# Performance work log

Hardware: AMD Instinct MI355X
Metric: run time of the kernel (lower is better)

## Reference

```python
import jax, jax.numpy as jnp
import numpy as np
from jax import lax

DECAY = 0.1
THRESH = 0.5
LENS = 1.0
D_IN = 2 * 34 * 34  # 2312
HID = 800
NC = 10

@jax.custom_vjp
def act_fun(x):
    return (x > THRESH).astype(x.dtype)

def _act_fwd(x):
    return act_fun(x), x

def _act_bwd(x, g):
    p = jax.nn.sigmoid((x - THRESH) / LENS)
    return (g * p * (1.0 - p) / LENS,)

act_fun.defvjp(_act_fwd, _act_bwd)


def setup_inputs() -> dict:
    key = jax.random.key(0)
    ks = jax.random.split(key, 8)
    B, T = 128, 300
    inp = jax.random.uniform(ks[0], (B, 2, 34, 34, 50), dtype=jnp.float32)
    X = jnp.zeros((B, 2, 34, 34, T), dtype=jnp.float32)
    idx = jax.random.randint(ks[1], (B,), 0, T - 50)
    W1 = jax.random.normal(ks[2], (HID, D_IN), dtype=jnp.float32) * 0.02
    b1 = jnp.zeros((HID,), dtype=jnp.float32)
    W2 = jax.random.normal(ks[3], (NC, HID), dtype=jnp.float32) * 0.03
    b2 = jnp.zeros((NC,), dtype=jnp.float32)
    Wc = jax.random.uniform(ks[4], (1, HID + 4), dtype=jnp.float32)  # ctrl init U(0,1)
    bc = jax.random.uniform(ks[5], (1,), dtype=jnp.float32)
    return {"input": inp, "X": X, "idx": idx, "W1": W1, "b1": b1,
            "W2": W2, "b2": b2, "Wc": Wc, "bc": bc}


def _paste(Xi, clip_i, idx_i):
    # X[i, :, :, :, idx:idx+50] = input[i].view(2,34,34,50)
    return lax.dynamic_update_slice(Xi, clip_i, (0, 0, 0, idx_i))


def reference(input, X, idx, W1, b1, W2, b2, Wc, bc):
    B = X.shape[0]
    T = X.shape[-1]
    X = jax.vmap(_paste)(X, input, idx.astype(jnp.int32))
    xs = jnp.moveaxis(X.reshape(B, D_IN, T), -1, 0)  # [T, B, D_IN]

    t = jnp.arange(T)
    freqs = jnp.stack([
        jnp.ones(T), (t % 2 == 0).astype(jnp.float32),
        (t % 10 == 0).astype(jnp.float32), (t % 100 == 0).astype(jnp.float32),
    ], axis=1).astype(X.dtype)  # [T, 4]
    is_first = (t == 0)

    f32 = X.dtype
    carry0 = (
        jnp.zeros((B, HID), f32), jnp.zeros((B, HID), f32),   # h1_mem, h1_spike
        jnp.zeros((B, NC), f32), jnp.zeros((B, NC), f32),     # h2_mem, h2_spike
        jnp.zeros((B, 1), f32), jnp.zeros((B, 1), f32),       # c_mem, c_spike
        jnp.ones((B, 1), f32), jnp.zeros((B, NC), f32),       # bgt, h2_sumspike
    )

    def step(carry, inps):
        h1m, h1s, h2m, h2s, cm, cs, bgt, sum2 = carry
        x, fq, first = inps
        x_a = jnp.where(first, x, x * cs)
        bgt = jnp.where(cs == 1.0, bgt + 1.0, bgt)
        h1m = h1m * DECAY * (1.0 - h1s) + x_a @ W1.T + b1
        h1s = act_fun(h1m)
        h2m = h2m * DECAY * (1.0 - h2s) + h1s @ W2.T + b2
        h2s = act_fun(h2m)
        c_in = jnp.concatenate(
            [lax.stop_gradient(h1s), jnp.broadcast_to(fq, (B, 4))], axis=1)
        cm = cm * 0.1 * (1.0 - cs) + c_in @ Wc.T + bc
        cs = act_fun(cm)
        sum2 = sum2 + h2s
        return (h1m, h1s, h2m, h2s, cm, cs, bgt, sum2), None

    carry, _ = lax.scan(step, carry0, (xs, freqs, is_first))
    bgt, sum2 = carry[6], carry[7]
    rate = sum2 / bgt
    return rate, X
```

## Files before the change

### kernel.cpp

```cpp
#include <hip/hip_runtime.h>

#define D_IN 2312
#define HID  800
#define NCLS 10
#define BATCH 128
#define TSTEPS 300
#define WIN  50

#define MT 64
#define NT 32
#define BKK 16
#define NTM 100
#define NTN 25
#define GEMM_BLOCKS (NTM * NTN)
#define BLK 128
#define RPASTE 1920
#define TOTQ (BATCH * D_IN * (TSTEPS / 4))

__global__ __launch_bounds__(BLK) void gemm_kernel(
    const float* __restrict__ inp,
    const float* __restrict__ W1,
    float*       __restrict__ P)
{
  __shared__ float As[BKK][MT];
  __shared__ float Bs[BKK][NT + 4];

  int t  = threadIdx.x;
  int bx = blockIdx.x;

  int mt = bx / NTN;
  int nt = bx - mt * NTN;
  int m0 = mt * MT, n0 = nt * NT;

  int am = t & 63;
  int ah = t >> 6;
  int r  = m0 + am;
  int bb = r / 50, ss = r - bb * 50;
  const float* aptr = inp + (size_t)bb * (D_IN * WIN) + ss;

  int bn = t >> 4;
  int bk = t & 15;

  int l  = t & 63;
  int lm = l & 7;
  int ln = l >> 3;
  int tm = ah * 32 + lm * 4;
  int tn = ln * 4;

  float aN[8], bN[4];
#pragma unroll
  for (int q = 0; q < 8; ++q) aN[q] = aptr[(ah * 8 + q) * WIN];
#pragma unroll
  for (int p = 0; p < 4; ++p)
    bN[p] = W1[(size_t)(n0 + bn + 8 * p) * D_IN + bk];

  float acc[4][4] = {};

  for (int k0 = 0; k0 < D_IN; k0 += BKK) {
#pragma unroll
    for (int q = 0; q < 8; ++q) As[ah * 8 + q][am] = aN[q];
#pragma unroll
    for (int p = 0; p < 4; ++p) Bs[bk][bn + 8 * p] = bN[p];
    __syncthreads();

    int kn0 = k0 + BKK;
    if (kn0 + BKK <= D_IN) {
#pragma unroll
      for (int q = 0; q < 8; ++q) aN[q] = aptr[(kn0 + ah * 8 + q) * WIN];
#pragma unroll
      for (int p = 0; p < 4; ++p)
        bN[p] = W1[(size_t)(n0 + bn + 8 * p) * D_IN + kn0 + bk];
    } else if (kn0 < D_IN) {
#pragma unroll
      for (int q = 0; q < 8; ++q) {
        int kk = kn0 + ah * 8 + q;
        aN[q] = (kk < D_IN) ? aptr[kk * WIN] : 0.f;
      }
#pragma unroll
      for (int p = 0; p < 4; ++p) {
        int kk = kn0 + bk;
        bN[p] = (kk < D_IN) ? W1[(size_t)(n0 + bn + 8 * p) * D_IN + kk] : 0.f;
      }
    }

#pragma unroll
    for (int kk = 0; kk < BKK; ++kk) {
      float4 A0 = *(const float4*)&As[kk][tm];
      float4 B0 = *(const float4*)&Bs[kk][tn];
      float av[4] = {A0.x, A0.y, A0.z, A0.w};
      float bv[4] = {B0.x, B0.y, B0.z, B0.w};
#pragma unroll
      for (int i = 0; i < 4; ++i)
#pragma unroll
        for (int j = 0; j < 4; ++j)
          acc[i][j] += av[i] * bv[j];
    }
    __syncthreads();
  }

#pragma unroll
  for (int i = 0; i < 4; ++i) {
    int row = m0 + tm + i;
    *(float4*)&P[(size_t)row * HID + n0 + tn] =
        make_float4(acc[i][0], acc[i][1], acc[i][2], acc[i][3]);
  }
}

template <int CTRL>
__device__ __forceinline__ float dpp_add(float s) {
  return s + __int_as_float(__builtin_amdgcn_update_dpp(
      0, __float_as_int(s), CTRL, 0xf, 0xf, true));
}
__device__ __forceinline__ float wave_sum(float s) {
  s = dpp_add<0x111>(s);
  s = dpp_add<0x112>(s);
  s = dpp_add<0x114>(s);
  s = dpp_add<0x118>(s);
  s = dpp_add<0x142>(s);
  s = dpp_add<0x143>(s);
  return __int_as_float(__builtin_amdgcn_readlane(__float_as_int(s), 63));
}

__global__ __launch_bounds__(64, 1) void recur_kernel(
    const float* __restrict__ P,
    const float* __restrict__ W2,
    const float* __restrict__ b2,
    const float* __restrict__ Wc,
    const float* __restrict__ bc,
    const float* __restrict__ b1,
    const int*   __restrict__ idx,
    float*       __restrict__ out,
    const float* __restrict__ inp,
    float*       __restrict__ outX)
{
  int L = threadIdx.x;
  int b = blockIdx.x;

  if (b >= BATCH) {
    int tid = (b - BATCH) * 64 + L;
    const int stride = RPASTE * 64;
    for (int i = tid; i < TOTQ; i += stride) {
      int q  = i % 75;
      int rd = i / 75;
      int bb = rd / D_IN;
      int d  = rd - bb * D_IN;
      int ib = idx[bb];
      const float* ip = inp + (size_t)bb * (D_IN * WIN) + (size_t)d * WIN;
      int t0 = q * 4;
      float v[4];
#pragma unroll
      for (int e = 0; e < 4; ++e) {
        unsigned w = (unsigned)(t0 + e - ib);
        v[e] = (w < (unsigned)WIN) ? ip[w] : 0.f;
      }
      *(float4*)&outX[(size_t)rd * TSTEPS + t0] = make_float4(v[0], v[1], v[2], v[3]);
    }
    return;
  }

  int myidx = idx[b];
  const float* Pb = P + (size_t)b * WIN * HID;

  float m[13], b1r[13], wcr[13];
  float w2r[NCLS][13];
  unsigned smask = 0;
#pragma unroll
  for (int rr = 0; rr < 13; ++rr) {
    int j = L + 64 * rr;
    bool ok = (j < HID);
    m[rr]   = 0.f;
    b1r[rr] = ok ? b1[j] : 0.f;
    wcr[rr] = ok ? Wc[j] : 0.f;
#pragma unroll
    for (int c = 0; c < NCLS; ++c)
      w2r[c][rr] = ok ? W2[c * HID + j] : 0.f;
  }

  float cm = 0.f, cs = 0.f, bgt = 1.f;
  float bc0 = bc[0];
  float wf0 = Wc[HID], wf1 = Wc[HID + 1], wf2 = Wc[HID + 2], wf3 = Wc[HID + 3];

  float h2m[10], h2s[10], sum2[10], b2r[10];
#pragma unroll
  for (int c = 0; c < NCLS; ++c) { h2m[c] = 0.f; h2s[c] = 0.f; sum2[c] = 0.f; b2r[c] = b2[c]; }

  float cur[13];
  {
    unsigned w0 = (unsigned)(0 - myidx);
    if (w0 < (unsigned)WIN) {
      const float* Pr = Pb + (size_t)w0 * HID;
#pragma unroll
      for (int rr = 0; rr < 13; ++rr) {
        int j = L + 64 * rr;
        cur[rr] = (j < HID) ? Pr[j] : 0.f;
      }
    } else {
#pragma unroll
      for (int rr = 0; rr < 13; ++rr) cur[rr] = 0.f;
    }
  }

  for (int step = 0; step < TSTEPS; ++step) {
    float gate = (step == 0) ? 1.f : cs;

    float nxt[13];
    {
      unsigned wn = (unsigned)(step + 1 - myidx);
      if (wn < (unsigned)WIN) {
        const float* Pr = Pb + (size_t)wn * HID;
#pragma unroll
        for (int rr = 0; rr < 13; ++rr) {
          int j = L + 64 * rr;
          nxt[rr] = (j < HID) ? Pr[j] : 0.f;
        }
      } else {
#pragma unroll
        for (int rr = 0; rr < 13; ++rr) nxt[rr] = 0.f;
      }
    }

    unsigned nmask = 0;
#pragma unroll
    for (int rr = 0; rr < 13; ++rr) {
      float mprev = ((smask >> rr) & 1u) ? 0.f : m[rr] * 0.1f;
      float mv = mprev + cur[rr] * gate + b1r[rr];
      m[rr] = mv;
      nmask |= (mv > 0.5f) ? (1u << rr) : 0u;
    }
    smask = nmask;

    unsigned long long ball = __ballot(smask != 0u);

    float ctrl = 0.f;
    float dot[10];
#pragma unroll
    for (int c = 0; c < NCLS; ++c) dot[c] = 0.f;

    if (ball) {
      float cacc = 0.f;
#pragma unroll
      for (int rr = 0; rr < 13; ++rr) {
        float f = (float)((smask >> rr) & 1u);
        cacc = fmaf(f, wcr[rr], cacc);
      }
      ctrl = wave_sum(cacc);

#pragma unroll
      for (int rr = 0; rr < 13; ++rr) {
        float f = (float)((smask >> rr) & 1u);
#pragma unroll
        for (int c = 0; c < NCLS; ++c)
          dot[c] = fmaf(f, w2r[c][rr], dot[c]);
      }
#pragma unroll
      for (int c = 0; c < NCLS; ++c) dot[c] = wave_sum(dot[c]);
    }

    bgt += (cs == 1.f) ? 1.f : 0.f;
    float fq = wf0;
    if ((step & 1) == 0)   fq += wf1;
    if (step % 10 == 0)    fq += wf2;
    if (step % 100 == 0)   fq += wf3;
    float cv = (cs != 0.f ? 0.f : cm * 0.1f) + ctrl + fq + bc0;
    cm = cv;
    cs = (cv > 0.5f) ? 1.f : 0.f;

#pragma unroll
    for (int c = 0; c < NCLS; ++c) {
      float v = (h2s[c] != 0.f ? 0.f : h2m[c] * 0.1f) + dot[c] + b2r[c];
      h2m[c] = v;
      h2s[c] = (v > 0.5f) ? 1.f : 0.f;
      sum2[c] += h2s[c];
    }

#pragma unroll
    for (int rr = 0; rr < 13; ++rr) cur[rr] = nxt[rr];
  }

  if (L == 0) {
#pragma unroll
    for (int c = 0; c < NCLS; ++c) out[b * NCLS + c] = sum2[c] / bgt;
  }
}

extern "C" void kernel_launch(void* const* d_in, const int* in_sizes, int n_in,
                              void* d_out, int out_size, void* d_ws, size_t ws_size,
                              hipStream_t stream) {
  const float* inp = (const float*)d_in[0];
  const int*   idx = (const int*)d_in[2];
  const float* W1  = (const float*)d_in[3];
  const float* b1  = (const float*)d_in[4];
  const float* W2  = (const float*)d_in[5];
  const float* b2  = (const float*)d_in[6];
  const float* Wc  = (const float*)d_in[7];
  const float* bc  = (const float*)d_in[8];

  float* out = (float*)d_out;
  float* P   = (float*)d_ws;

  gemm_kernel<<<GEMM_BLOCKS, BLK, 0, stream>>>(inp, W1, P);

  recur_kernel<<<BATCH + RPASTE, 64, 0, stream>>>(
      P, W2, b2, Wc, bc, b1, idx, out, inp, out + BATCH * NCLS);
}
```

Baseline: 1.032 ms.

## Prefetch recurrence inputs two steps ahead and remap GEMM blocks per XCD

The recurrence loop now keeps two register buffers and issues the load of P for step+2 right after the membrane update consumes the current buffer, so each global load has about two steps of latency to hide instead of one. The loop is unrolled by two through a macro. Separately, GEMM block indices are remapped so that consecutive logical tiles land on the same XCD, which should improve L2 reuse of the A and W1 tiles. The trade-off is higher register pressure in the single-wave recurrence kernel.

```diff
diff --git a/kernel.cpp b/kernel.cpp
--- a/kernel.cpp
+++ b/kernel.cpp
@@ -25,8 +25,14 @@
   __shared__ float As[BKK][MT];
   __shared__ float Bs[BKK][NT + 4];
 
-  int t  = threadIdx.x;
-  int bx = blockIdx.x;
+  int t   = threadIdx.x;
+  int bx0 = blockIdx.x;
+
+  int xcd = bx0 & 7;
+  int jj  = bx0 >> 3;
+  const int q8 = GEMM_BLOCKS >> 3;
+  const int r8 = GEMM_BLOCKS & 7;
+  int bx = (xcd < r8 ? xcd * (q8 + 1) : r8 * (q8 + 1) + (xcd - r8) * q8) + jj;
 
   int mt = bx / NTN;
   int nt = bx - mt * NTN;
@@ -120,6 +126,73 @@
   s = dpp_add<0x143>(s);
   return __int_as_float(__builtin_amdgcn_readlane(__float_as_int(s), 63));
 }
+
+#define STEP_BODY(S, BUF)                                                    \
+  {                                                                          \
+    float gate = ((S) == 0) ? 1.f : cs;                                      \
+    unsigned nmask = 0;                                                      \
+    _Pragma("unroll")                                                        \
+    for (int rr = 0; rr < 13; ++rr) {                                        \
+      float mprev = ((smask >> rr) & 1u) ? 0.f : m[rr] * 0.1f;               \
+      float mv = mprev + BUF[rr] * gate + b1r[rr];                           \
+      m[rr] = mv;                                                            \
+      nmask |= (mv > 0.5f) ? (1u << rr) : 0u;                                \
+    }                                                                        \
+    smask = nmask;                                                           \
+     \
+    {                                                                        \
+      unsigned wn = (unsigned)((S) + 2 - myidx);                             \
+      if (wn < (unsigned)WIN) {                                              \
+        const float* Pr = Pb + (size_t)wn * HID;                             \
+        _Pragma("unroll")                                                    \
+        for (int rr = 0; rr < 13; ++rr) {                                    \
+          int j = L + 64 * rr;                                               \
+          BUF[rr] = (j < HID) ? Pr[j] : 0.f;                                 \
+        }                                                                    \
+      } else {                                                               \
+        _Pragma("unroll")                                                    \
+        for (int rr = 0; rr < 13; ++rr) BUF[rr] = 0.f;                       \
+      }                                                                      \
+    }                                                                        \
+    unsigned long long ball = __ballot(smask != 0u);                         \
+    float ctrl = 0.f;                                                        \
+    float dot[10];                                                           \
+    _Pragma("unroll")                                                        \
+    for (int c = 0; c < NCLS; ++c) dot[c] = 0.f;                             \
+    if (ball) {                                                              \
+      float cacc = 0.f;                                                      \
+      _Pragma("unroll")                                                      \
+      for (int rr = 0; rr < 13; ++rr) {                                      \
+        float f = (float)((smask >> rr) & 1u);                               \
+        cacc = fmaf(f, wcr[rr], cacc);                                       \
+      }                                                                      \
+      ctrl = wave_sum(cacc);                                                 \
+      _Pragma("unroll")                                                      \
+      for (int rr = 0; rr < 13; ++rr) {                                      \
+        float f = (float)((smask >> rr) & 1u);                               \
+        _Pragma("unroll")                                                    \
+        for (int c = 0; c < NCLS; ++c)                                       \
+          dot[c] = fmaf(f, w2r[c][rr], dot[c]);                              \
+      }                                                                      \
+      _Pragma("unroll")                                                      \
+      for (int c = 0; c < NCLS; ++c) dot[c] = wave_sum(dot[c]);              \
+    }                                                                        \
+    bgt += (cs == 1.f) ? 1.f : 0.f;                                          \
+    float fq = wf0;                                                          \
+    if (((S) & 1) == 0)    fq += wf1;                                        \
+    if ((S) % 10 == 0)     fq += wf2;                                        \
+    if ((S) % 100 == 0)    fq += wf3;                                        \
+    float cv = (cs != 0.f ? 0.f : cm * 0.1f) + ctrl + fq + bc0;              \
+    cm = cv;                                                                 \
+    cs = (cv > 0.5f) ? 1.f : 0.f;                                            \
+    _Pragma("unroll")                                                        \
+    for (int c = 0; c < NCLS; ++c) {                                         \
+      float v = (h2s[c] != 0.f ? 0.f : h2m[c] * 0.1f) + dot[c] + b2r[c];     \
+      h2m[c] = v;                                                            \
+      h2s[c] = (v > 0.5f) ? 1.f : 0.f;                                       \
+      sum2[c] += h2s[c];                                                     \
+    }                                                                        \
+  }
 
 __global__ __launch_bounds__(64, 1) void recur_kernel(
     const float* __restrict__ P,
@@ -184,7 +257,9 @@
 #pragma unroll
   for (int c = 0; c < NCLS; ++c) { h2m[c] = 0.f; h2s[c] = 0.f; sum2[c] = 0.f; b2r[c] = b2[c]; }
 
-  float cur[13];
+  float bufA[13], bufB[13];
+#pragma unroll
+  for (int rr = 0; rr < 13; ++rr) { bufA[rr] = 0.f; bufB[rr] = 0.f; }
   {
     unsigned w0 = (unsigned)(0 - myidx);
     if (w0 < (unsigned)WIN) {
@@ -192,89 +267,23 @@
 #pragma unroll
       for (int rr = 0; rr < 13; ++rr) {
         int j = L + 64 * rr;
-        cur[rr] = (j < HID) ? Pr[j] : 0.f;
-      }
-    } else {
-#pragma unroll
-      for (int rr = 0; rr < 13; ++rr) cur[rr] = 0.f;
-    }
-  }
-
-  for (int step = 0; step < TSTEPS; ++step) {
-    float gate = (step == 0) ? 1.f : cs;
-
-    float nxt[13];
-    {
-      unsigned wn = (unsigned)(step + 1 - myidx);
-      if (wn < (unsigned)WIN) {
-        const float* Pr = Pb + (size_t)wn * HID;
-#pragma unroll
-        for (int rr = 0; rr < 13; ++rr) {
-          int j = L + 64 * rr;
-          nxt[rr] = (j < HID) ? Pr[j] : 0.f;
-        }
-      } else {
-#pragma unroll
-        for (int rr = 0; rr < 13; ++rr) nxt[rr] = 0.f;
-      }
-    }
-
-    unsigned nmask = 0;
-#pragma unroll
-    for (int rr = 0; rr < 13; ++rr) {
-      float mprev = ((smask >> rr) & 1u) ? 0.f : m[rr] * 0.1f;
-      float mv = mprev + cur[rr] * gate + b1r[rr];
-      m[rr] = mv;
-      nmask |= (mv > 0.5f) ? (1u << rr) : 0u;
-    }
-    smask = nmask;
-
-    unsigned long long ball = __ballot(smask != 0u);
-
-    float ctrl = 0.f;
-    float dot[10];
-#pragma unroll
-    for (int c = 0; c < NCLS; ++c) dot[c] = 0.f;
-
-    if (ball) {
-      float cacc = 0.f;
+        bufA[rr] = (j < HID) ? Pr[j] : 0.f;
+      }
+    }
+    unsigned w1 = (unsigned)(1 - myidx);
+    if (w1 < (unsigned)WIN) {
+      const float* Pr = Pb + (size_t)w1 * HID;
 #pragma unroll
       for (int rr = 0; rr < 13; ++rr) {
-        float f = (float)((smask >> rr) & 1u);
-        cacc = fmaf(f, wcr[rr], cacc);
-      }
-      ctrl = wave_sum(cacc);
-
-#pragma unroll
-      for (int rr = 0; rr < 13; ++rr) {
-        float f = (float)((smask >> rr) & 1u);
-#pragma unroll
-        for (int c = 0; c < NCLS; ++c)
-          dot[c] = fmaf(f, w2r[c][rr], dot[c]);
-      }
-#pragma unroll
-      for (int c = 0; c < NCLS; ++c) dot[c] = wave_sum(dot[c]);
-    }
-
-    bgt += (cs == 1.f) ? 1.f : 0.f;
-    float fq = wf0;
-    if ((step & 1) == 0)   fq += wf1;
-    if (step % 10 == 0)    fq += wf2;
-    if (step % 100 == 0)   fq += wf3;
-    float cv = (cs != 0.f ? 0.f : cm * 0.1f) + ctrl + fq + bc0;
-    cm = cv;
-    cs = (cv > 0.5f) ? 1.f : 0.f;
-
-#pragma unroll
-    for (int c = 0; c < NCLS; ++c) {
-      float v = (h2s[c] != 0.f ? 0.f : h2m[c] * 0.1f) + dot[c] + b2r[c];
-      h2m[c] = v;
-      h2s[c] = (v > 0.5f) ? 1.f : 0.f;
-      sum2[c] += h2s[c];
-    }
-
-#pragma unroll
-    for (int rr = 0; rr < 13; ++rr) cur[rr] = nxt[rr];
+        int j = L + 64 * rr;
+        bufB[rr] = (j < HID) ? Pr[j] : 0.f;
+      }
+    }
+  }
+
+  for (int step = 0; step < TSTEPS; step += 2) {
+    STEP_BODY(step,     bufA);
+    STEP_BODY(step + 1, bufB);
   }
 
   if (L == 0) {
```

Result: slower. 1.084 ms (+5.1%).
